# Optimization experiments

Measured on AMD Instinct MI355X. Metric: run time of the kernel, lower is better.

Reference implementation:

```python
import jax, jax.numpy as jnp
import numpy as np

B, C, H, W = 8, 1152, 32, 32
N = H * W


def _skew(t):
    # t: (B,3) -> (B,3,3) skew-symmetric
    z = jnp.zeros_like(t[:, 0])
    return jnp.stack([
        jnp.stack([z, -t[:, 2], t[:, 1]], axis=-1),
        jnp.stack([t[:, 2], z, -t[:, 0]], axis=-1),
        jnp.stack([-t[:, 1], t[:, 0], z], axis=-1),
    ], axis=1)


def _fundamental(K1, K2, R, t):
    E = _skew(t) @ R
    U, S, Vt = jnp.linalg.svd(E)
    S = S.at[:, 2].set(0.0)  # enforce rank-2 essential matrix
    E = U @ (S[:, :, None] * Vt)
    return jnp.linalg.inv(jnp.swapaxes(K2, 1, 2)) @ E @ jnp.linalg.inv(K1)


def setup_inputs() -> dict:
    key = jax.random.key(0)
    k1, k2, k3, k4, k5 = jax.random.split(key, 5)
    f_tar = jax.random.normal(k1, (B, C, H, W), dtype=jnp.float32)
    f_src = jax.random.normal(k2, (B, C, H, W), dtype=jnp.float32)
    # realistic invertible intrinsics: [[fx,0,cx],[0,fy,cy],[0,0,1]]
    def intrinsics(k):
        f = 30.0 + 2.0 * jax.random.uniform(k, (B, 2))
        Kt = jnp.zeros((B, 3, 3))
        Kt = Kt.at[:, 0, 0].set(f[:, 0]).at[:, 1, 1].set(f[:, 1])
        Kt = Kt.at[:, 0, 2].set(W / 2.0).at[:, 1, 2].set(H / 2.0).at[:, 2, 2].set(1.0)
        return Kt.astype(jnp.float32)
    K1 = intrinsics(k3)
    K2 = intrinsics(k4)
    # proper rotation via QR of a random matrix
    ka, kb = jax.random.split(k5)
    Q, Rm = jnp.linalg.qr(jax.random.normal(ka, (B, 3, 3)))
    Q = Q * jnp.sign(jnp.diagonal(Rm, axis1=1, axis2=2))[:, None, :]
    Q = Q * jnp.linalg.det(Q)[:, None, None]  # det = +1
    t = jax.random.normal(kb, (B, 3), dtype=jnp.float32)
    return {"f_tar": f_tar, "f_src": f_src, "K1": K1, "K2": K2,
            "R": Q.astype(jnp.float32), "t": t}


def reference(f_tar, f_src, K1, K2, R, t):
    f_src_flat = f_src.reshape(B, C, N)  # (B,C,N)
    # NOTE: torch code computes A = f_src^T @ f_tar but never uses it (dead code); omitted.

    # homogeneous pixel coords, indexing='ij': x=row index, y=col index
    ix, iy = jnp.meshgrid(jnp.arange(H, dtype=jnp.float32),
                          jnp.arange(W, dtype=jnp.float32), indexing='ij')
    combined = jnp.stack([ix.ravel(), iy.ravel(), jnp.ones(N, jnp.float32)], axis=0)  # (3,N)
    combined = jnp.broadcast_to(combined, (B, 3, N))

    F_mat = _fundamental(K1, K2, R, t)                       # (B,3,3)
    lines = F_mat @ combined                                 # (B,3,N)
    lines = lines / lines[:, 2:3, :]

    ones = jnp.ones((B, 1, N), jnp.float32)
    x0 = jnp.zeros((B, 1, N), jnp.float32)
    y0 = -lines[:, 2:3, :] / lines[:, 1:2, :]
    point_0 = jnp.concatenate([x0, y0, ones], axis=1)        # (B,3,N)
    x1 = jnp.full((B, 1, N), float(W), jnp.float32)
    y1 = -(lines[:, 2:3, :] + lines[:, 0:1, :] * W) / lines[:, 1:2, :]
    point_1 = jnp.concatenate([x1, y1, ones], axis=1)        # (B,3,N)

    # point-to-line distance for every (pixel i, line j) pair -> (B,N,N)
    diff = point_0 - point_1                                 # (B,3,N)
    p = combined[:, :, :, None] - point_0[:, :, None, :]     # (B,3,N,N) via broadcast
    d = diff[:, :, None, :]                                  # (B,3,1,N)
    cross = jnp.stack([
        p[:, 1] * d[:, 2] - p[:, 2] * d[:, 1],
        p[:, 2] * d[:, 0] - p[:, 0] * d[:, 2],
        p[:, 0] * d[:, 1] - p[:, 1] * d[:, 0],
    ], axis=1)                                               # (B,3,N,N)
    cross_norm = jnp.sqrt(jnp.sum(cross * cross, axis=1))    # (B,N,N)
    diff_norm = jnp.linalg.norm(diff, axis=1, keepdims=True) # (B,1,N)
    d_epi = cross_norm / diff_norm                           # (B,N,N)

    thre = 0.1
    weight_map = 1.0 - jax.nn.softmax(5.0 * (d_epi - thre), axis=-1)
    attention_map = jax.nn.softmax(weight_map, axis=1)       # softmax over dim=1, per torch code

    out = jnp.einsum('bij,bjc->bic', attention_map, jnp.swapaxes(f_src_flat, 1, 2))  # (B,N,C)
    return out.reshape(B, C, H, W)
```

## Files before the change

### kernel.cpp

```cpp
#include <hip/hip_runtime.h>
#include <hip/hip_bf16.h>
#include <math.h>

#define Bn 8
#define Cn 1152
#define Nn 1024

typedef short short8 __attribute__((ext_vector_type(8)));
typedef float f32x4 __attribute__((ext_vector_type(4)));

__device__ float g_csum_part[Bn * 32 * Nn];
__device__ float g_icsum[Bn * Nn];
__device__ unsigned short g_A[(size_t)Bn * Nn * Nn];

__device__ inline unsigned short f2bf(float x) {
    __hip_bfloat16 h = __float2bfloat16(x);
    unsigned short u;
    __builtin_memcpy(&u, &h, 2);
    return u;
}

__device__ inline void inv3(const float* M, float* o) {
    float a = M[0], b = M[1], c = M[2];
    float d = M[3], e = M[4], f = M[5];
    float g = M[6], h = M[7], i = M[8];
    float A0 = (e * i - f * h);
    float A1 = -(d * i - f * g);
    float A2 = (d * h - e * g);
    float det = a * A0 + b * A1 + c * A2;
    float inv = 1.0f / det;
    o[0] = A0 * inv;
    o[1] = -(b * i - c * h) * inv;
    o[2] = (b * f - c * e) * inv;
    o[3] = A1 * inv;
    o[4] = (a * i - c * g) * inv;
    o[5] = -(a * f - c * d) * inv;
    o[6] = A2 * inv;
    o[7] = -(a * h - b * g) * inv;
    o[8] = (a * e - b * d) * inv;
}

__device__ inline void mm3(const float* X, const float* Y, float* Z) {
    for (int r = 0; r < 3; r++)
        for (int c = 0; c < 3; c++)
            Z[r * 3 + c] = X[r * 3 + 0] * Y[0 * 3 + c] + X[r * 3 + 1] * Y[1 * 3 + c] +
                           X[r * 3 + 2] * Y[2 * 3 + c];
}

__device__ inline void computeF(const float* K1, const float* K2, const float* R,
                                const float* t, int b, float* F) {
    float t0 = t[b * 3 + 0], t1 = t[b * 3 + 1], t2 = t[b * 3 + 2];
    float S[9] = {0.0f, -t2, t1, t2, 0.0f, -t0, -t1, t0, 0.0f};
    float E[9];
    mm3(S, &R[b * 9], E);
    float iK1[9], iK2[9];
    inv3(&K1[b * 9], iK1);
    inv3(&K2[b * 9], iK2);
    float iK2T[9] = {iK2[0], iK2[3], iK2[6], iK2[1], iK2[4], iK2[7], iK2[2], iK2[5], iK2[8]};
    float T[9];
    mm3(iK2T, E, T);
    mm3(T, iK1, F);
}

__device__ inline float4 zcoef(const float* F, int j) {
    float jx = (float)(j >> 5);
    float jy = (float)(j & 31);
    float l0 = F[0] * jx + F[1] * jy + F[2];
    float l1 = F[3] * jx + F[4] * jy + F[5];
    float l2 = F[6] * jx + F[7] * jy + F[8];
    l0 = l0 / l2;
    l1 = l1 / l2;
    float y0 = -1.0f / l1;
    float y1 = -(1.0f + l0 * 32.0f) / l1;
    float dy = y0 - y1;
    float invn = 1.0f / sqrtf(1024.0f + dy * dy);
    return make_float4(5.0f * dy * invn, 160.0f * invn, 160.0f * y0 * invn, 0.0f);
}

__launch_bounds__(256) __global__ void fusedE_kernel(const float* __restrict__ K1,
                                                     const float* __restrict__ K2,
                                                     const float* __restrict__ R,
                                                     const float* __restrict__ t) {
    __shared__ float Fs[9];
    __shared__ float4 prm[Nn];
    __shared__ float red[4][16][64];
    int lin = blockIdx.x;
    int b = lin & 7;
    int seg = lin >> 3;
    if (threadIdx.x == 0) computeF(K1, K2, R, t, b, Fs);
    __syncthreads();
#pragma unroll
    for (int u = 0; u < 4; u++) {
        int j = threadIdx.x * 4 + u;
        prm[j] = zcoef(Fs, j);
    }
    __syncthreads();
    int wv = threadIdx.x >> 6;
    int lane = threadIdx.x & 63;
    float px[16], py[16], pz[16];
#pragma unroll
    for (int k = 0; k < 16; k++) {
        float4 p = prm[lane + k * 64];
        px[k] = p.x;
        py[k] = p.y;
        pz[k] = p.z;
    }
    float csum[16];
#pragma unroll
    for (int k = 0; k < 16; k++) csum[k] = 0.0f;
#pragma unroll
    for (int rr = 0; rr < 8; rr++) {
        int i = seg * 32 + wv * 8 + rr;
        float ix = (float)(i >> 5), iy = (float)(i & 31);
        float e[16], m = -INFINITY;
#pragma unroll
        for (int k = 0; k < 16; k++) {
            e[k] = fabsf(fmaf(ix, px[k], fmaf(iy, py[k], -pz[k]))) - 0.5f;
            m = fmaxf(m, e[k]);
        }
#pragma unroll
        for (int o = 32; o > 0; o >>= 1) m = fmaxf(m, __shfl_xor(m, o, 64));
        float s = 0.0f;
#pragma unroll
        for (int k = 0; k < 16; k++) {
            e[k] = __expf(e[k] - m);
            s += e[k];
        }
#pragma unroll
        for (int o = 32; o > 0; o >>= 1) s += __shfl_xor(s, o, 64);
        float rsi = 1.0f / s;
        unsigned short* arow = g_A + (size_t)(b * Nn + i) * Nn;
#pragma unroll
        for (int k = 0; k < 16; k++) {
            float E = __expf(1.0f - e[k] * rsi);
            csum[k] += E;
            arow[lane + k * 64] = f2bf(E);
        }
    }
#pragma unroll
    for (int k = 0; k < 16; k++) red[wv][k][lane] = csum[k];
    __syncthreads();
    int l2 = threadIdx.x & 63;
    int k0 = (threadIdx.x >> 6) * 4;
#pragma unroll
    for (int q = 0; q < 4; q++) {
        int k = k0 + q;
        float ssum = red[0][k][l2] + red[1][k][l2] + red[2][k][l2] + red[3][k][l2];
        g_csum_part[(b * 32 + seg) * Nn + k * 64 + l2] = ssum;
    }
}

__global__ void icsum_kernel() {
    int b = blockIdx.x;
    int j0 = threadIdx.x * 4;
    float4 cs = *(const float4*)&g_csum_part[(b * 32 + 0) * Nn + j0];
#pragma unroll
    for (int it = 1; it < 32; it++) {
        float4 p = *(const float4*)&g_csum_part[(b * 32 + it) * Nn + j0];
        cs.x += p.x; cs.y += p.y; cs.z += p.z; cs.w += p.w;
    }
    float4 inv = make_float4(1.0f / cs.x, 1.0f / cs.y, 1.0f / cs.z, 1.0f / cs.w);
    *(float4*)&g_icsum[b * Nn + j0] = inv;
}

#define BM 128
#define BNc 64
#define BK 32

__launch_bounds__(256, 4) __global__ void gemm_kernel(const float* __restrict__ fsrc,
                                                      float* __restrict__ out) {
    __shared__ unsigned short As[2][BM * BK];
    __shared__ unsigned short Bs[2][BNc * BK];
    __shared__ float ics[Nn];
    int lin = blockIdx.x;
    int b = lin & 7;
    int s = lin >> 3;
    int it = s & 7;
    int ct = s >> 3;
    int i0 = it * BM;
    int c0 = ct * BNc;
    int t = threadIdx.x;
    int w = t >> 6, L = t & 63;
    int wr = w >> 1, wc = w & 1;
    const unsigned short* Ab = g_A + (size_t)b * Nn * Nn + (size_t)i0 * Nn;
    const float* Fb = fsrc + ((size_t)b * Cn + c0) * Nn;

#pragma unroll
    for (int u = 0; u < 4; u++) {
        int j = t + u * 256;
        ics[j] = g_icsum[b * Nn + j];
    }

    auto stage = [&](int p, int kt) {
#pragma unroll
        for (int h = 0; h < 2; h++) {
            int chunk = h * 256 + t;
            int rr = chunk >> 2;
            int gq = (chunk & 3) ^ ((rr >> 1) & 3);
            const unsigned short* ga = Ab + (size_t)rr * Nn + kt + gq * 8;
            __builtin_amdgcn_global_load_lds(
                (const __attribute__((address_space(1))) unsigned int*)ga,
                (__attribute__((address_space(3))) unsigned int*)(As[p] + chunk * 8), 16, 0, 0);
        }
        {
            int chunk = t;
            int rr = chunk >> 2;
            int gq = (chunk & 3) ^ ((rr >> 1) & 3);
            const float* gb = Fb + (size_t)rr * Nn + kt + gq * 8;
            float4 v0 = *(const float4*)gb;
            float4 v1 = *(const float4*)(gb + 4);
            const float* icp = &ics[kt + gq * 8];
            ushort4 u0, u1;
            u0.x = f2bf(v0.x * icp[0]);
            u0.y = f2bf(v0.y * icp[1]);
            u0.z = f2bf(v0.z * icp[2]);
            u0.w = f2bf(v0.w * icp[3]);
            u1.x = f2bf(v1.x * icp[4]);
            u1.y = f2bf(v1.y * icp[5]);
            u1.z = f2bf(v1.z * icp[6]);
            u1.w = f2bf(v1.w * icp[7]);
            *(ushort4*)(Bs[p] + chunk * 8) = u0;
            *(ushort4*)(Bs[p] + chunk * 8 + 4) = u1;
        }
    };

    f32x4 acc[4][2] = {};
    int lrow = L & 15, quad = L >> 4;
    __syncthreads();
    stage(0, 0);
    for (int kt = 0; kt < Nn; kt += BK) {
        int p = (kt >> 5) & 1;
        __syncthreads();
        if (kt + BK < Nn) stage(1 - p, kt + BK);
        short8 af[4], bf[2];
#pragma unroll
        for (int mt = 0; mt < 4; mt++) {
            int rr = wr * 64 + mt * 16 + lrow;
            int q = quad ^ ((rr >> 1) & 3);
            af[mt] = *(const short8*)(As[p] + rr * BK + q * 8);
        }
#pragma unroll
        for (int nt = 0; nt < 2; nt++) {
            int cc = wc * 32 + nt * 16 + lrow;
            int q = quad ^ ((cc >> 1) & 3);
            bf[nt] = *(const short8*)(Bs[p] + cc * BK + q * 8);
        }
#pragma unroll
        for (int mt = 0; mt < 4; mt++)
#pragma unroll
            for (int nt = 0; nt < 2; nt++)
                acc[mt][nt] =
                    __builtin_amdgcn_mfma_f32_16x16x32_bf16(af[mt], bf[nt], acc[mt][nt], 0, 0, 0);
    }
    int col = L & 15;
#pragma unroll
    for (int mt = 0; mt < 4; mt++)
#pragma unroll
        for (int rg = 0; rg < 4; rg++) {
            int i = i0 + wr * 64 + mt * 16 + quad * 4 + rg;
            float* orow = out + ((size_t)b * Nn + i) * Cn + c0 + wc * 32;
#pragma unroll
            for (int nt = 0; nt < 2; nt++) orow[nt * 16 + col] = acc[mt][nt][rg];
        }
}

extern "C" void kernel_launch(void* const* d_in, const int* in_sizes, int n_in,
                              void* d_out, int out_size, void* d_ws, size_t ws_size,
                              hipStream_t stream) {
    (void)in_sizes; (void)n_in; (void)d_ws; (void)ws_size; (void)out_size;
    const float* f_src = (const float*)d_in[1];
    const float* K1 = (const float*)d_in[2];
    const float* K2 = (const float*)d_in[3];
    const float* R = (const float*)d_in[4];
    const float* t = (const float*)d_in[5];
    float* out = (float*)d_out;

    fusedE_kernel<<<dim3(256), dim3(256), 0, stream>>>(K1, K2, R, t);
    icsum_kernel<<<dim3(8), dim3(256), 0, stream>>>();
    gemm_kernel<<<dim3(Bn * (Nn / BM) * (Cn / BNc)), dim3(256), 0, stream>>>(f_src, out);
}
```

Baseline: 185.1 us.

## Fuse three kernels into one persistent kernel with software grid barriers

Merges the epipolar attention-weight kernel, the column-sum inverse kernel and the bf16 GEMM into one launch of 1152 blocks that are separated by atomic grid barriers. The weight phase spreads over 1024 blocks instead of 256, and the column-sum reduction is spread over 256 blocks. The GEMM loop now issues the B-operand global loads before the MFMAs and converts/writes them after, to hide load latency. It removes two launch gaps and raises parallelism in the first phase, but relies on all 1152 blocks being co-resident (launch bounds raised to 5 blocks per CU) and adds barrier spin cost.

```diff
diff --git a/kernel.cpp b/kernel.cpp
--- a/kernel.cpp
+++ b/kernel.cpp
@@ -5,13 +5,36 @@
 #define Bn 8
 #define Cn 1152
 #define Nn 1024
+#define GRID 1152
 
 typedef short short8 __attribute__((ext_vector_type(8)));
 typedef float f32x4 __attribute__((ext_vector_type(4)));
 
-__device__ float g_csum_part[Bn * 32 * Nn];
-__device__ float g_icsum[Bn * Nn];
+__device__ float g_csp[Bn * 128 * Nn];
+__device__ float g_ics[Bn * Nn];
 __device__ unsigned short g_A[(size_t)Bn * Nn * Nn];
+
+__device__ unsigned g_bar_count = 0;
+__device__ unsigned g_bar_gen = 0;
+
+__device__ inline void grid_barrier() {
+    __syncthreads();
+    if (threadIdx.x == 0) {
+        __threadfence();
+        unsigned gen = __hip_atomic_load(&g_bar_gen, __ATOMIC_ACQUIRE, __HIP_MEMORY_SCOPE_AGENT);
+        unsigned arr =
+            __hip_atomic_fetch_add(&g_bar_count, 1u, __ATOMIC_ACQ_REL, __HIP_MEMORY_SCOPE_AGENT);
+        if (arr + 1u == (unsigned)GRID) {
+            __hip_atomic_store(&g_bar_count, 0u, __ATOMIC_RELAXED, __HIP_MEMORY_SCOPE_AGENT);
+            __hip_atomic_fetch_add(&g_bar_gen, 1u, __ATOMIC_RELEASE, __HIP_MEMORY_SCOPE_AGENT);
+        } else {
+            while (__hip_atomic_load(&g_bar_gen, __ATOMIC_ACQUIRE, __HIP_MEMORY_SCOPE_AGENT) ==
+                   gen)
+                __builtin_amdgcn_s_sleep(1);
+        }
+    }
+    __syncthreads();
+}
 
 __device__ inline unsigned short f2bf(float x) {
     __hip_bfloat16 h = __float2bfloat16(x);
@@ -77,191 +100,202 @@
     return make_float4(5.0f * dy * invn, 160.0f * invn, 160.0f * y0 * invn, 0.0f);
 }
 
-__launch_bounds__(256) __global__ void fusedE_kernel(const float* __restrict__ K1,
-                                                     const float* __restrict__ K2,
-                                                     const float* __restrict__ R,
-                                                     const float* __restrict__ t) {
-    __shared__ float Fs[9];
-    __shared__ float4 prm[Nn];
-    __shared__ float red[4][16][64];
-    int lin = blockIdx.x;
-    int b = lin & 7;
-    int seg = lin >> 3;
-    if (threadIdx.x == 0) computeF(K1, K2, R, t, b, Fs);
-    __syncthreads();
-#pragma unroll
-    for (int u = 0; u < 4; u++) {
-        int j = threadIdx.x * 4 + u;
-        prm[j] = zcoef(Fs, j);
-    }
-    __syncthreads();
-    int wv = threadIdx.x >> 6;
-    int lane = threadIdx.x & 63;
-    float px[16], py[16], pz[16];
-#pragma unroll
-    for (int k = 0; k < 16; k++) {
-        float4 p = prm[lane + k * 64];
-        px[k] = p.x;
-        py[k] = p.y;
-        pz[k] = p.z;
-    }
-    float csum[16];
-#pragma unroll
-    for (int k = 0; k < 16; k++) csum[k] = 0.0f;
-#pragma unroll
-    for (int rr = 0; rr < 8; rr++) {
-        int i = seg * 32 + wv * 8 + rr;
-        float ix = (float)(i >> 5), iy = (float)(i & 31);
-        float e[16], m = -INFINITY;
-#pragma unroll
-        for (int k = 0; k < 16; k++) {
-            e[k] = fabsf(fmaf(ix, px[k], fmaf(iy, py[k], -pz[k]))) - 0.5f;
-            m = fmaxf(m, e[k]);
-        }
-#pragma unroll
-        for (int o = 32; o > 0; o >>= 1) m = fmaxf(m, __shfl_xor(m, o, 64));
-        float s = 0.0f;
-#pragma unroll
-        for (int k = 0; k < 16; k++) {
-            e[k] = __expf(e[k] - m);
-            s += e[k];
-        }
-#pragma unroll
-        for (int o = 32; o > 0; o >>= 1) s += __shfl_xor(s, o, 64);
-        float rsi = 1.0f / s;
-        unsigned short* arow = g_A + (size_t)(b * Nn + i) * Nn;
-#pragma unroll
-        for (int k = 0; k < 16; k++) {
-            float E = __expf(1.0f - e[k] * rsi);
-            csum[k] += E;
-            arow[lane + k * 64] = f2bf(E);
-        }
-    }
-#pragma unroll
-    for (int k = 0; k < 16; k++) red[wv][k][lane] = csum[k];
-    __syncthreads();
-    int l2 = threadIdx.x & 63;
-    int k0 = (threadIdx.x >> 6) * 4;
-#pragma unroll
-    for (int q = 0; q < 4; q++) {
-        int k = k0 + q;
-        float ssum = red[0][k][l2] + red[1][k][l2] + red[2][k][l2] + red[3][k][l2];
-        g_csum_part[(b * 32 + seg) * Nn + k * 64 + l2] = ssum;
-    }
-}
-
-__global__ void icsum_kernel() {
-    int b = blockIdx.x;
-    int j0 = threadIdx.x * 4;
-    float4 cs = *(const float4*)&g_csum_part[(b * 32 + 0) * Nn + j0];
-#pragma unroll
-    for (int it = 1; it < 32; it++) {
-        float4 p = *(const float4*)&g_csum_part[(b * 32 + it) * Nn + j0];
-        cs.x += p.x; cs.y += p.y; cs.z += p.z; cs.w += p.w;
-    }
-    float4 inv = make_float4(1.0f / cs.x, 1.0f / cs.y, 1.0f / cs.z, 1.0f / cs.w);
-    *(float4*)&g_icsum[b * Nn + j0] = inv;
-}
-
 #define BM 128
 #define BNc 64
 #define BK 32
 
-__launch_bounds__(256, 4) __global__ void gemm_kernel(const float* __restrict__ fsrc,
-                                                      float* __restrict__ out) {
-    __shared__ unsigned short As[2][BM * BK];
-    __shared__ unsigned short Bs[2][BNc * BK];
-    __shared__ float ics[Nn];
+__launch_bounds__(256, 5) __global__ void mega_kernel(
+    const float* __restrict__ K1, const float* __restrict__ K2, const float* __restrict__ R,
+    const float* __restrict__ t, const float* __restrict__ fsrc, float* __restrict__ out) {
+    __shared__ __align__(16) char smem[28672];
     int lin = blockIdx.x;
+    int tid = threadIdx.x;
     int b = lin & 7;
-    int s = lin >> 3;
-    int it = s & 7;
-    int ct = s >> 3;
-    int i0 = it * BM;
-    int c0 = ct * BNc;
-    int t = threadIdx.x;
-    int w = t >> 6, L = t & 63;
-    int wr = w >> 1, wc = w & 1;
-    const unsigned short* Ab = g_A + (size_t)b * Nn * Nn + (size_t)i0 * Nn;
-    const float* Fb = fsrc + ((size_t)b * Cn + c0) * Nn;
-
-#pragma unroll
-    for (int u = 0; u < 4; u++) {
-        int j = t + u * 256;
-        ics[j] = g_icsum[b * Nn + j];
+
+    if (lin < 1024) {
+        float* prmx = (float*)smem;
+        float* prmy = (float*)(smem + 4096);
+        float* prmz = (float*)(smem + 8192);
+        float* Fs = (float*)(smem + 12288);
+        float(*red)[16][64] = (float(*)[16][64])(smem + 12288);
+        int seg = lin >> 3;
+        if (tid == 0) computeF(K1, K2, R, t, b, Fs);
+        __syncthreads();
+#pragma unroll
+        for (int u = 0; u < 4; u++) {
+            int j = tid * 4 + u;
+            float4 p = zcoef(Fs, j);
+            prmx[j] = p.x;
+            prmy[j] = p.y;
+            prmz[j] = p.z;
+        }
+        __syncthreads();
+        int wv = tid >> 6, lane = tid & 63;
+#pragma unroll
+        for (int rr = 0; rr < 2; rr++) {
+            int i = seg * 8 + wv * 2 + rr;
+            float ix = (float)(i >> 5), iy = (float)(i & 31);
+            float e[16], m = -INFINITY;
+#pragma unroll
+            for (int k = 0; k < 16; k++) {
+                int j = lane + k * 64;
+                e[k] = fabsf(fmaf(ix, prmx[j], fmaf(iy, prmy[j], -prmz[j]))) - 0.5f;
+                m = fmaxf(m, e[k]);
+            }
+#pragma unroll
+            for (int o = 32; o > 0; o >>= 1) m = fmaxf(m, __shfl_xor(m, o, 64));
+            float s = 0.0f;
+#pragma unroll
+            for (int k = 0; k < 16; k++) {
+                e[k] = __expf(e[k] - m);
+                s += e[k];
+            }
+#pragma unroll
+            for (int o = 32; o > 0; o >>= 1) s += __shfl_xor(s, o, 64);
+            float rsi = 1.0f / s;
+            unsigned short* arow = g_A + (size_t)(b * Nn + i) * Nn;
+#pragma unroll
+            for (int k = 0; k < 16; k++) {
+                float E = __expf(1.0f - e[k] * rsi);
+                arow[lane + k * 64] = f2bf(E);
+                if (rr == 0)
+                    red[wv][k][lane] = E;
+                else
+                    red[wv][k][lane] += E;
+            }
+        }
+        __syncthreads();
+        int l2 = tid & 63, k0 = (tid >> 6) * 4;
+#pragma unroll
+        for (int q = 0; q < 4; q++) {
+            int k = k0 + q;
+            float ssum = red[0][k][l2] + red[1][k][l2] + red[2][k][l2] + red[3][k][l2];
+            g_csp[((size_t)(b * 128 + seg)) * Nn + k * 64 + l2] = ssum;
+        }
     }
-
-    auto stage = [&](int p, int kt) {
-#pragma unroll
-        for (int h = 0; h < 2; h++) {
-            int chunk = h * 256 + t;
-            int rr = chunk >> 2;
-            int gq = (chunk & 3) ^ ((rr >> 1) & 3);
-            const unsigned short* ga = Ab + (size_t)rr * Nn + kt + gq * 8;
-            __builtin_amdgcn_global_load_lds(
-                (const __attribute__((address_space(1))) unsigned int*)ga,
-                (__attribute__((address_space(3))) unsigned int*)(As[p] + chunk * 8), 16, 0, 0);
-        }
-        {
-            int chunk = t;
-            int rr = chunk >> 2;
-            int gq = (chunk & 3) ^ ((rr >> 1) & 3);
-            const float* gb = Fb + (size_t)rr * Nn + kt + gq * 8;
-            float4 v0 = *(const float4*)gb;
-            float4 v1 = *(const float4*)(gb + 4);
-            const float* icp = &ics[kt + gq * 8];
+    grid_barrier();
+
+    if (lin < 256) {
+        float* red2 = (float*)smem;
+        int jl = tid & 31, sg = tid >> 5;
+        int jbase = (lin >> 3) * 32;
+        const float* base = g_csp + (size_t)b * 128 * Nn + jbase + jl;
+        float sum = 0.0f;
+#pragma unroll
+        for (int u = 0; u < 16; u++) sum += base[(size_t)(sg * 16 + u) * Nn];
+        red2[tid] = sum;
+        __syncthreads();
+        if (tid < 32) {
+            float ssum = red2[tid];
+#pragma unroll
+            for (int g2 = 1; g2 < 8; g2++) ssum += red2[g2 * 32 + tid];
+            g_ics[b * Nn + jbase + tid] = 1.0f / ssum;
+        }
+    }
+    grid_barrier();
+
+    {
+        unsigned short* As0 = (unsigned short*)smem;
+        unsigned short* Bs0 = (unsigned short*)(smem + 16384);
+        float* ics = (float*)(smem + 24576);
+        int sblk = lin >> 3;
+        int it = sblk & 7;
+        int ct = sblk >> 3;
+        int i0 = it * BM;
+        int c0 = ct * BNc;
+        int w = tid >> 6, L = tid & 63;
+        int wr = w >> 1, wc = w & 1;
+        const unsigned short* Ab = g_A + (size_t)b * Nn * Nn + (size_t)i0 * Nn;
+        const float* Fb = fsrc + ((size_t)b * Cn + c0) * Nn;
+
+#pragma unroll
+        for (int u = 0; u < 4; u++) {
+            int j = tid + u * 256;
+            ics[j] = g_ics[b * Nn + j];
+        }
+        __syncthreads();
+
+        int chunkB = tid;
+        int rrB = chunkB >> 2;
+        int gqB = (chunkB & 3) ^ ((rrB >> 1) & 3);
+        const float* gB = Fb + (size_t)rrB * Nn + gqB * 8;
+        float4 bv0, bv1;
+        auto loadB = [&](int kt) {
+            bv0 = *(const float4*)(gB + kt);
+            bv1 = *(const float4*)(gB + kt + 4);
+        };
+        auto writeB = [&](int p, int kt) {
+            const float* icp = &ics[kt + gqB * 8];
             ushort4 u0, u1;
-            u0.x = f2bf(v0.x * icp[0]);
-            u0.y = f2bf(v0.y * icp[1]);
-            u0.z = f2bf(v0.z * icp[2]);
-            u0.w = f2bf(v0.w * icp[3]);
-            u1.x = f2bf(v1.x * icp[4]);
-            u1.y = f2bf(v1.y * icp[5]);
-            u1.z = f2bf(v1.z * icp[6]);
-            u1.w = f2bf(v1.w * icp[7]);
-            *(ushort4*)(Bs[p] + chunk * 8) = u0;
-            *(ushort4*)(Bs[p] + chunk * 8 + 4) = u1;
-        }
-    };
-
-    f32x4 acc[4][2] = {};
-    int lrow = L & 15, quad = L >> 4;
-    __syncthreads();
-    stage(0, 0);
-    for (int kt = 0; kt < Nn; kt += BK) {
-        int p = (kt >> 5) & 1;
-        __syncthreads();
-        if (kt + BK < Nn) stage(1 - p, kt + BK);
-        short8 af[4], bf[2];
-#pragma unroll
-        for (int mt = 0; mt < 4; mt++) {
-            int rr = wr * 64 + mt * 16 + lrow;
-            int q = quad ^ ((rr >> 1) & 3);
-            af[mt] = *(const short8*)(As[p] + rr * BK + q * 8);
-        }
-#pragma unroll
-        for (int nt = 0; nt < 2; nt++) {
-            int cc = wc * 32 + nt * 16 + lrow;
-            int q = quad ^ ((cc >> 1) & 3);
-            bf[nt] = *(const short8*)(Bs[p] + cc * BK + q * 8);
-        }
+            u0.x = f2bf(bv0.x * icp[0]);
+            u0.y = f2bf(bv0.y * icp[1]);
+            u0.z = f2bf(bv0.z * icp[2]);
+            u0.w = f2bf(bv0.w * icp[3]);
+            u1.x = f2bf(bv1.x * icp[4]);
+            u1.y = f2bf(bv1.y * icp[5]);
+            u1.z = f2bf(bv1.z * icp[6]);
+            u1.w = f2bf(bv1.w * icp[7]);
+            *(ushort4*)(Bs0 + p * 2048 + chunkB * 8) = u0;
+            *(ushort4*)(Bs0 + p * 2048 + chunkB * 8 + 4) = u1;
+        };
+        auto stageA = [&](int p, int kt) {
+#pragma unroll
+            for (int h = 0; h < 2; h++) {
+                int chunk = h * 256 + tid;
+                int rr = chunk >> 2;
+                int gq = (chunk & 3) ^ ((rr >> 1) & 3);
+                const unsigned short* ga = Ab + (size_t)rr * Nn + kt + gq * 8;
+                __builtin_amdgcn_global_load_lds(
+                    (const __attribute__((address_space(1))) unsigned int*)ga,
+                    (__attribute__((address_space(3))) unsigned int*)(As0 + p * 4096 + chunk * 8),
+                    16, 0, 0);
+            }
+        };
+
+        f32x4 acc[4][2] = {};
+        int lrow = L & 15, quad = L >> 4;
+        loadB(0);
+        stageA(0, 0);
+        writeB(0, 0);
+        for (int kt = 0; kt < Nn; kt += BK) {
+            int p = (kt >> 5) & 1;
+            __syncthreads();
+            if (kt + BK < Nn) {
+                loadB(kt + BK);
+                stageA(1 - p, kt + BK);
+            }
+            short8 af[4], bf[2];
+#pragma unroll
+            for (int mt = 0; mt < 4; mt++) {
+                int rr2 = wr * 64 + mt * 16 + lrow;
+                int q = quad ^ ((rr2 >> 1) & 3);
+                af[mt] = *(const short8*)(As0 + p * 4096 + rr2 * BK + q * 8);
+            }
+#pragma unroll
+            for (int nt = 0; nt < 2; nt++) {
+                int cc = wc * 32 + nt * 16 + lrow;
+                int q = quad ^ ((cc >> 1) & 3);
+                bf[nt] = *(const short8*)(Bs0 + p * 2048 + cc * BK + q * 8);
+            }
+#pragma unroll
+            for (int mt = 0; mt < 4; mt++)
+#pragma unroll
+                for (int nt = 0; nt < 2; nt++)
+                    acc[mt][nt] = __builtin_amdgcn_mfma_f32_16x16x32_bf16(af[mt], bf[nt],
+                                                                          acc[mt][nt], 0, 0, 0);
+            if (kt + BK < Nn) writeB(1 - p, kt + BK);
+        }
+        int col = L & 15;
 #pragma unroll
         for (int mt = 0; mt < 4; mt++)
 #pragma unroll
-            for (int nt = 0; nt < 2; nt++)
-                acc[mt][nt] =
-                    __builtin_amdgcn_mfma_f32_16x16x32_bf16(af[mt], bf[nt], acc[mt][nt], 0, 0, 0);
+            for (int rg = 0; rg < 4; rg++) {
+                int i = i0 + wr * 64 + mt * 16 + quad * 4 + rg;
+                float* orow = out + ((size_t)b * Nn + i) * Cn + c0 + wc * 32;
+#pragma unroll
+                for (int nt = 0; nt < 2; nt++) orow[nt * 16 + col] = acc[mt][nt][rg];
+            }
     }
-    int col = L & 15;
-#pragma unroll
-    for (int mt = 0; mt < 4; mt++)
-#pragma unroll
-        for (int rg = 0; rg < 4; rg++) {
-            int i = i0 + wr * 64 + mt * 16 + quad * 4 + rg;
-            float* orow = out + ((size_t)b * Nn + i) * Cn + c0 + wc * 32;
-#pragma unroll
-            for (int nt = 0; nt < 2; nt++) orow[nt * 16 + col] = acc[mt][nt][rg];
-        }
 }
 
 extern "C" void kernel_launch(void* const* d_in, const int* in_sizes, int n_in,
@@ -275,7 +309,5 @@
     const float* t = (const float*)d_in[5];
     float* out = (float*)d_out;
 
-    fusedE_kernel<<<dim3(256), dim3(256), 0, stream>>>(K1, K2, R, t);
-    icsum_kernel<<<dim3(8), dim3(256), 0, stream>>>();
-    gemm_kernel<<<dim3(Bn * (Nn / BM) * (Cn / BNc)), dim3(256), 0, stream>>>(f_src, out);
-}
+    mega_kernel<<<dim3(GRID), dim3(256), 0, stream>>>(K1, K2, R, t, f_src, out);
+}
```

Result: slower. 533.7 us (+188.4%).
